# Kernel optimization log

Measured on AMD Instinct MI355X. Metric: run time of the kernel, lower is better.

The kernel has to match this reference:

```python
import jax, jax.numpy as jnp
import numpy as np

N_NODES = 100000
N_EDGES = 800000
NODE_IN = 32
EDGE_DIM = 84
HIDDEN = 24
HEAD_HIDDEN = 20
DEPTH = 2
CAT = 2 * HIDDEN + EDGE_DIM  # 132
LN_EPS = 1e-5


def _gelu(x):
    # torch nn.GELU default = exact erf form
    return jax.nn.gelu(x, approximate=False)


def _ln(x, g, b):
    m = jnp.mean(x, axis=-1, keepdims=True)
    v = jnp.var(x, axis=-1, keepdims=True)
    return (x - m) * jax.lax.rsqrt(v + LN_EPS) * g + b


def setup_inputs() -> dict:
    key = jax.random.key(0)
    ks = jax.random.split(key, 32)
    f = jnp.float32

    def nrm(k, shape, scale=0.05):
        return jax.random.normal(k, shape, dtype=f) * scale

    inp = {
        "x": jax.random.normal(ks[0], (N_NODES, NODE_IN), dtype=f),
        "edge_attr": jax.random.normal(ks[1], (N_EDGES, EDGE_DIM), dtype=f),
        # input projection
        "node_w": nrm(ks[2], (NODE_IN, HIDDEN)),
        "node_b": jnp.zeros((HIDDEN,), f),
        # intrinsic head
        "ih_w1": nrm(ks[3], (HIDDEN, HEAD_HIDDEN)),
        "ih_b1": jnp.zeros((HEAD_HIDDEN,), f),
        "ih_w2": nrm(ks[4], (HEAD_HIDDEN, 1)),
        "ih_b2": jnp.zeros((1,), f),
        # per-layer phi_e (stacked over depth)
        "pe_w1": nrm(ks[5], (DEPTH, CAT, EDGE_DIM)),
        "pe_b1": jnp.zeros((DEPTH, EDGE_DIM), f),
        "pe_w2": nrm(ks[6], (DEPTH, EDGE_DIM, EDGE_DIM)),
        "pe_b2": jnp.zeros((DEPTH, EDGE_DIM), f),
        # per-layer phi_v
        "pv_w1": nrm(ks[7], (DEPTH, CAT, HIDDEN)),
        "pv_b1": jnp.zeros((DEPTH, HIDDEN), f),
        "pv_w2": nrm(ks[8], (DEPTH, HIDDEN, HIDDEN)),
        "pv_b2": jnp.zeros((DEPTH, HIDDEN), f),
        # layer norms
        "ne_g": jnp.ones((DEPTH, EDGE_DIM), f),
        "ne_b": jnp.zeros((DEPTH, EDGE_DIM), f),
        "nv_g": jnp.ones((DEPTH, HIDDEN), f),
        "nv_b": jnp.zeros((DEPTH, HIDDEN), f),
        # context head
        "ch_w1": nrm(ks[9], (HIDDEN, HEAD_HIDDEN)),
        "ch_b1": jnp.zeros((HEAD_HIDDEN,), f),
        "ch_w2": nrm(ks[10], (HEAD_HIDDEN, 1)),
        "ch_b2": jnp.zeros((1,), f),
        "mu": jnp.zeros((), f),
        "edge_index": jax.random.randint(ks[11], (2, N_EDGES), 0, N_NODES),
    }
    return inp


def reference(x, edge_attr, node_w, node_b, ih_w1, ih_b1, ih_w2, ih_b2,
              pe_w1, pe_b1, pe_w2, pe_b2, pv_w1, pv_b1, pv_w2, pv_b2,
              ne_g, ne_b, nv_g, nv_b, ch_w1, ch_b1, ch_w2, ch_b2, mu,
              edge_index):
    src, dst = edge_index[0], edge_index[1]
    n = x.shape[0]
    # eval mode: dropout and edge_drop are inactive
    h = x @ node_w + node_b                                   # [N, H]
    intrinsic = (_gelu(h @ ih_w1 + ih_b1) @ ih_w2 + ih_b2)[:, 0]
    e = edge_attr                                             # [E, De]
    ones = jnp.ones((src.shape[0], 1), dtype=x.dtype)
    counts = jnp.maximum(jax.ops.segment_sum(ones, dst, num_segments=n), 1.0)
    for i in range(DEPTH):
        hs, hd = h[src], h[dst]                               # gathers [E, H]
        cat = jnp.concatenate([hs, hd, e], axis=-1)           # [E, 132]
        e_msg = _gelu(cat @ pe_w1[i] + pe_b1[i]) @ pe_w2[i] + pe_b2[i]
        e = _ln(e + e_msg, ne_g[i], ne_b[i])
        cat = jnp.concatenate([hs, hd, e], axis=-1)
        m = _gelu(cat @ pv_w1[i] + pv_b1[i]) @ pv_w2[i] + pv_b2[i]
        agg = jax.ops.segment_sum(m, dst, num_segments=n) / counts  # scatter-mean
        h = _ln(h + agg, nv_g[i], nv_b[i])
    context = (_gelu(h @ ch_w1 + ch_b1) @ ch_w2 + ch_b2)[:, 0]
    return mu + intrinsic + context
```

## Files before the change

### kernel.cpp

```cpp
#include <hip/hip_runtime.h>
#include <math.h>

#define N_NODES 100000
#define N_EDGES 800000
#define NODE_IN 32
#define EDGE_DIM 84
#define HIDDEN 24
#define HEAD_HIDDEN 20
#define CAT_DIM 132
#define LN_EPS 1e-5f

typedef __attribute__((ext_vector_type(8))) short short8;
typedef __attribute__((ext_vector_type(4))) float f32x4;
typedef unsigned int uint;
typedef unsigned short ushort;

__device__ __forceinline__ float gelu_exact(float x) {
    return 0.5f * x * (1.0f + erff(x * 0.70710678118654752f));
}
__device__ __forceinline__ ushort f2bf(float f) {
    union { float f; uint u; } c; c.f = f;
    uint u = c.u;
    return (ushort)((u + 0x7fffu + ((u >> 16) & 1u)) >> 16);
}
__device__ __forceinline__ float bf2f(ushort s) {
    union { uint u; float f; } c; c.u = ((uint)s) << 16; return c.f;
}

__global__ void k_prep_w(const float* __restrict__ pe_w1, const float* __restrict__ pe_w2,
                         const float* __restrict__ pv_w1, const float* __restrict__ pv_w2,
                         ushort* __restrict__ wp) {
    int idx = blockIdx.x * 256 + threadIdx.x;
    int j = idx & 7;
    int lane = (idx >> 3) & 63;
    int frag = idx >> 9;
    int kq = (lane >> 4) * 8 + j;
    int n15 = lane & 15;
    float v = 0.f;
    if (frag < 60) {
        int l = frag / 30, f = frag % 30;
        int kt = f / 6, nt = f % 6;
        int k = kt * 32 + kq, n = nt * 16 + n15;
        if (k < CAT_DIM && n < EDGE_DIM) v = pe_w1[(l * CAT_DIM + k) * EDGE_DIM + n];
    } else if (frag < 96) {
        int f2 = frag - 60; int l = f2 / 18, f = f2 % 18;
        int kt = f / 6, nt = f % 6;
        int k = kt * 32 + kq, n = nt * 16 + n15;
        if (k < EDGE_DIM && n < EDGE_DIM) v = pe_w2[(l * EDGE_DIM + k) * EDGE_DIM + n];
    } else if (frag < 116) {
        int f2 = frag - 96; int l = f2 / 10, f = f2 % 10;
        int kt = f / 2, nt = f % 2;
        int k = kt * 32 + kq, n = nt * 16 + n15;
        if (k < CAT_DIM && n < HIDDEN) v = pv_w1[(l * CAT_DIM + k) * HIDDEN + n];
    } else {
        int f2 = frag - 116; int l = f2 / 2, nt = f2 % 2;
        int k = kq, n = nt * 16 + n15;
        if (k < HIDDEN && n < HIDDEN) v = pv_w2[(l * HIDDEN + k) * HIDDEN + n];
    }
    wp[idx] = f2bf(v);
}

__global__ void k_node_in(const float* __restrict__ x,
                          const float* __restrict__ node_w, const float* __restrict__ node_b,
                          const float* __restrict__ ih_w1, const float* __restrict__ ih_b1,
                          const float* __restrict__ ih_w2, const float* __restrict__ ih_b2,
                          float* __restrict__ h, ushort* __restrict__ h_bf,
                          float* __restrict__ intr) {
    int n = blockIdx.x * blockDim.x + threadIdx.x;
    if (n >= N_NODES) return;
    float xv[NODE_IN];
    const float4* xp = (const float4*)(x + (size_t)n * NODE_IN);
#pragma unroll
    for (int i = 0; i < NODE_IN / 4; i++) {
        float4 v = xp[i];
        xv[4*i+0] = v.x; xv[4*i+1] = v.y; xv[4*i+2] = v.z; xv[4*i+3] = v.w;
    }
    float hv[HIDDEN];
#pragma unroll
    for (int j = 0; j < HIDDEN; j++) hv[j] = node_b[j];
    for (int k = 0; k < NODE_IN; k++) {
        float xk = xv[k];
#pragma unroll
        for (int j = 0; j < HIDDEN; j++) hv[j] = fmaf(xk, node_w[k * HIDDEN + j], hv[j]);
    }
#pragma unroll
    for (int j = 0; j < HIDDEN; j++) {
        h[(size_t)n * HIDDEN + j] = hv[j];
        h_bf[(size_t)n * HIDDEN + j] = f2bf(hv[j]);
    }
    float acc = ih_b2[0];
    for (int j = 0; j < HEAD_HIDDEN; j++) {
        float t = ih_b1[j];
#pragma unroll
        for (int k = 0; k < HIDDEN; k++) t = fmaf(hv[k], ih_w1[k * HEAD_HIDDEN + j], t);
        acc = fmaf(gelu_exact(t), ih_w2[j], acc);
    }
    intr[n] = acc;
}

__global__ void k_counts(const int* __restrict__ ei, int* __restrict__ cnt) {
    int e = blockIdx.x * blockDim.x + threadIdx.x;
    if (e >= N_EDGES) return;
    atomicAdd(&cnt[ei[N_EDGES + e]], 1);
}

__global__ __launch_bounds__(256, 2)
void k_edge_e(const ushort* __restrict__ h_bf,
              const float* __restrict__ e_in_f32,
              ushort* __restrict__ e_bf,
              const int* __restrict__ ei,
              const ushort* __restrict__ w1f, const ushort* __restrict__ w2f,
              const float* __restrict__ b1, const float* __restrict__ b2,
              const float* __restrict__ g, const float* __restrict__ bb) {
    __shared__ __align__(16) uint sA32[128 * 84];
    __shared__ __align__(16) ushort sT[128 * 104];
    __shared__ int s_idx[256];

    const int tid = threadIdx.x;
    const int e0 = blockIdx.x * 128;
    s_idx[tid] = ei[(size_t)(tid >> 7) * N_EDGES + e0 + (tid & 127)];
    __syncthreads();

    {
        int e = tid >> 1, hf = tid & 1;
        int src = s_idx[e], dst = s_idx[128 + e];
        const uint* hb = (const uint*)h_bf;
        uint* row = sA32 + e * 84;
#pragma unroll
        for (int i = 0; i < 6; i++) row[hf * 6 + i] = hb[src * 12 + hf * 6 + i];
#pragma unroll
        for (int i = 0; i < 6; i++) row[12 + hf * 6 + i] = hb[dst * 12 + hf * 6 + i];
        if (e_in_f32) {
            const float* er = e_in_f32 + (size_t)(e0 + e) * 84;
#pragma unroll
            for (int i = 0; i < 21; i++) {
                int jd = hf * 21 + i;
                uint lo = f2bf(er[2 * jd]), hi = f2bf(er[2 * jd + 1]);
                row[24 + jd] = lo | (hi << 16);
            }
        } else {
            const uint* er = (const uint*)e_bf + (size_t)(e0 + e) * 42;
#pragma unroll
            for (int i = 0; i < 21; i++) { int jd = hf * 21 + i; row[24 + jd] = er[jd]; }
        }
#pragma unroll
        for (int i = 0; i < 7; i++) row[66 + hf * 7 + i] = 0u;
    }

    const int lane = tid & 63, wave = tid >> 6;
    const int quad = lane >> 4, l15 = lane & 15;
    float b1v[6], b2v[6], gv[6], bbv[6];
#pragma unroll
    for (int nt = 0; nt < 6; nt++) {
        int col = nt * 16 + l15;
        bool ok = col < EDGE_DIM;
        b1v[nt] = ok ? b1[col] : 0.f;
        b2v[nt] = ok ? b2[col] : 0.f;
        gv[nt]  = ok ? g[col]  : 0.f;
        bbv[nt] = ok ? bb[col] : 0.f;
    }
    __syncthreads();

    const ushort* sAu = (const ushort*)sA32;
    const int r0 = wave * 32 + l15;

    f32x4 acc[2][6];
#pragma unroll
    for (int mt = 0; mt < 2; mt++)
#pragma unroll
        for (int nt = 0; nt < 6; nt++) acc[mt][nt] = (f32x4)0.f;

#pragma unroll
    for (int kt = 0; kt < 5; kt++) {
        short8 a0 = *(const short8*)(sAu + (size_t)r0 * 168 + kt * 32 + quad * 8);
        short8 a1 = *(const short8*)(sAu + (size_t)(r0 + 16) * 168 + kt * 32 + quad * 8);
        const short8* bp = (const short8*)w1f + kt * 6 * 64 + lane;
#pragma unroll
        for (int nt = 0; nt < 6; nt++) {
            short8 b = bp[nt * 64];
            acc[0][nt] = __builtin_amdgcn_mfma_f32_16x16x32_bf16(a0, b, acc[0][nt], 0, 0, 0);
            acc[1][nt] = __builtin_amdgcn_mfma_f32_16x16x32_bf16(a1, b, acc[1][nt], 0, 0, 0);
        }
    }

#pragma unroll
    for (int mt = 0; mt < 2; mt++)
#pragma unroll
        for (int nt = 0; nt < 6; nt++)
#pragma unroll
            for (int r = 0; r < 4; r++) {
                int row = wave * 32 + mt * 16 + quad * 4 + r;
                sT[row * 104 + nt * 16 + l15] = f2bf(gelu_exact(acc[mt][nt][r] + b1v[nt]));
            }
    __syncthreads();

    f32x4 acc2[2][6];
#pragma unroll
    for (int mt = 0; mt < 2; mt++)
#pragma unroll
        for (int nt = 0; nt < 6; nt++) acc2[mt][nt] = (f32x4)0.f;

#pragma unroll
    for (int kt = 0; kt < 3; kt++) {
        short8 a0 = *(const short8*)(sT + (size_t)r0 * 104 + kt * 32 + quad * 8);
        short8 a1 = *(const short8*)(sT + (size_t)(r0 + 16) * 104 + kt * 32 + quad * 8);
        const short8* bp = (const short8*)w2f + kt * 6 * 64 + lane;
#pragma unroll
        for (int nt = 0; nt < 6; nt++) {
            short8 b = bp[nt * 64];
            acc2[0][nt] = __builtin_amdgcn_mfma_f32_16x16x32_bf16(a0, b, acc2[0][nt], 0, 0, 0);
            acc2[1][nt] = __builtin_amdgcn_mfma_f32_16x16x32_bf16(a1, b, acc2[1][nt], 0, 0, 0);
        }
    }

#pragma unroll
    for (int mt = 0; mt < 2; mt++) {
#pragma unroll
        for (int r = 0; r < 4; r++) {
            int row = wave * 32 + mt * 16 + quad * 4 + r;
            float ss = 0.f, qq = 0.f;
#pragma unroll
            for (int nt = 0; nt < 6; nt++) {
                int col = nt * 16 + l15;
                float v = acc2[mt][nt][r] + b2v[nt];
                if (col < EDGE_DIM) v += bf2f(sAu[row * 168 + 48 + col]);
                else v = 0.f;
                acc2[mt][nt][r] = v;
                ss += v;
                qq = fmaf(v, v, qq);
            }
            ss += __shfl_xor(ss, 1); ss += __shfl_xor(ss, 2);
            ss += __shfl_xor(ss, 4); ss += __shfl_xor(ss, 8);
            qq += __shfl_xor(qq, 1); qq += __shfl_xor(qq, 2);
            qq += __shfl_xor(qq, 4); qq += __shfl_xor(qq, 8);
            float mean = ss * (1.f / EDGE_DIM);
            float var  = qq * (1.f / EDGE_DIM) - mean * mean;
            float rstd = rsqrtf(var + LN_EPS);
#pragma unroll
            for (int nt = 0; nt < 6; nt++) {
                int col = nt * 16 + l15;
                if (col < EDGE_DIM) {
                    float o = (acc2[mt][nt][r] - mean) * rstd * gv[nt] + bbv[nt];
                    ((ushort*)sA32)[row * 168 + 48 + col] = f2bf(o);
                }
            }
        }
    }
    __syncthreads();

    uint* dst32 = (uint*)e_bf + (size_t)e0 * 42;
#pragma unroll
    for (int i = 0; i < 21; i++) {
        int idx = tid + 256 * i;
        int row = idx / 42, d = idx - row * 42;
        dst32[idx] = sA32[row * 84 + 24 + d];
    }
}

__global__ __launch_bounds__(256, 2)
void k_edge_v(const ushort* __restrict__ h_bf, const ushort* __restrict__ e_bf,
              const int* __restrict__ ei,
              const ushort* __restrict__ v1f, const ushort* __restrict__ v2f,
              const float* __restrict__ vb1, const float* __restrict__ vb2,
              float* __restrict__ agg) {
    __shared__ __align__(16) uint sA32[128 * 84];
    __shared__ __align__(16) ushort sT[128 * 40];
    __shared__ int s_idx[256];

    const int tid = threadIdx.x;
    const int e0 = blockIdx.x * 128;
    s_idx[tid] = ei[(size_t)(tid >> 7) * N_EDGES + e0 + (tid & 127)];
    __syncthreads();

    {
        int e = tid >> 1, hf = tid & 1;
        int src = s_idx[e], dst = s_idx[128 + e];
        const uint* hb = (const uint*)h_bf;
        uint* row = sA32 + e * 84;
#pragma unroll
        for (int i = 0; i < 6; i++) row[hf * 6 + i] = hb[src * 12 + hf * 6 + i];
#pragma unroll
        for (int i = 0; i < 6; i++) row[12 + hf * 6 + i] = hb[dst * 12 + hf * 6 + i];
        const uint* er = (const uint*)e_bf + (size_t)(e0 + e) * 42;
#pragma unroll
        for (int i = 0; i < 21; i++) { int jd = hf * 21 + i; row[24 + jd] = er[jd]; }
#pragma unroll
        for (int i = 0; i < 7; i++) row[66 + hf * 7 + i] = 0u;
    }

    const int lane = tid & 63, wave = tid >> 6;
    const int quad = lane >> 4, l15 = lane & 15;
    float vb1v[2], vb2v[2];
#pragma unroll
    for (int nt = 0; nt < 2; nt++) {
        int col = nt * 16 + l15;
        bool ok = col < HIDDEN;
        vb1v[nt] = ok ? vb1[col] : 0.f;
        vb2v[nt] = ok ? vb2[col] : 0.f;
    }
    __syncthreads();

    const ushort* sAu = (const ushort*)sA32;
    const int r0 = wave * 32 + l15;

    f32x4 acc[2][2];
#pragma unroll
    for (int mt = 0; mt < 2; mt++)
#pragma unroll
        for (int nt = 0; nt < 2; nt++) acc[mt][nt] = (f32x4)0.f;

#pragma unroll
    for (int kt = 0; kt < 5; kt++) {
        short8 a0 = *(const short8*)(sAu + (size_t)r0 * 168 + kt * 32 + quad * 8);
        short8 a1 = *(const short8*)(sAu + (size_t)(r0 + 16) * 168 + kt * 32 + quad * 8);
        const short8* bp = (const short8*)v1f + kt * 2 * 64 + lane;
#pragma unroll
        for (int nt = 0; nt < 2; nt++) {
            short8 b = bp[nt * 64];
            acc[0][nt] = __builtin_amdgcn_mfma_f32_16x16x32_bf16(a0, b, acc[0][nt], 0, 0, 0);
            acc[1][nt] = __builtin_amdgcn_mfma_f32_16x16x32_bf16(a1, b, acc[1][nt], 0, 0, 0);
        }
    }

#pragma unroll
    for (int mt = 0; mt < 2; mt++)
#pragma unroll
        for (int nt = 0; nt < 2; nt++)
#pragma unroll
            for (int r = 0; r < 4; r++) {
                int row = wave * 32 + mt * 16 + quad * 4 + r;
                sT[row * 40 + nt * 16 + l15] = f2bf(gelu_exact(acc[mt][nt][r] + vb1v[nt]));
            }
    __syncthreads();

    f32x4 acc2[2][2];
#pragma unroll
    for (int mt = 0; mt < 2; mt++)
#pragma unroll
        for (int nt = 0; nt < 2; nt++) acc2[mt][nt] = (f32x4)0.f;
    {
        short8 a0 = *(const short8*)(sT + (size_t)r0 * 40 + quad * 8);
        short8 a1 = *(const short8*)(sT + (size_t)(r0 + 16) * 40 + quad * 8);
        const short8* bp = (const short8*)v2f + lane;
#pragma unroll
        for (int nt = 0; nt < 2; nt++) {
            short8 b = bp[nt * 64];
            acc2[0][nt] = __builtin_amdgcn_mfma_f32_16x16x32_bf16(a0, b, acc2[0][nt], 0, 0, 0);
            acc2[1][nt] = __builtin_amdgcn_mfma_f32_16x16x32_bf16(a1, b, acc2[1][nt], 0, 0, 0);
        }
    }

#pragma unroll
    for (int mt = 0; mt < 2; mt++)
#pragma unroll
        for (int nt = 0; nt < 2; nt++) {
            int col = nt * 16 + l15;
            if (col < HIDDEN) {
#pragma unroll
                for (int r = 0; r < 4; r++) {
                    int row = wave * 32 + mt * 16 + quad * 4 + r;
                    int dst = s_idx[128 + row];
                    atomicAdd(&agg[(size_t)dst * HIDDEN + col], acc2[mt][nt][r] + vb2v[nt]);
                }
            }
        }
}

__global__ void k_node_up(float* __restrict__ h, ushort* __restrict__ h_bf,
                          const float* __restrict__ agg,
                          const int* __restrict__ cnt,
                          const float* __restrict__ g, const float* __restrict__ b) {
    int n = blockIdx.x * blockDim.x + threadIdx.x;
    if (n >= N_NODES) return;
    int c = cnt[n]; if (c < 1) c = 1;
    float inv = 1.0f / (float)c;
    float v[HIDDEN];
    float s = 0.f;
#pragma unroll
    for (int j = 0; j < HIDDEN; j++) {
        v[j] = h[(size_t)n * HIDDEN + j] + agg[(size_t)n * HIDDEN + j] * inv;
        s += v[j];
    }
    float mean = s * (1.f / HIDDEN);
    float sq = 0.f;
#pragma unroll
    for (int j = 0; j < HIDDEN; j++) { float d = v[j] - mean; sq = fmaf(d, d, sq); }
    float rstd = rsqrtf(sq * (1.f / HIDDEN) + LN_EPS);
#pragma unroll
    for (int j = 0; j < HIDDEN; j++) {
        float o = (v[j] - mean) * rstd * g[j] + b[j];
        h[(size_t)n * HIDDEN + j] = o;
        h_bf[(size_t)n * HIDDEN + j] = f2bf(o);
    }
}

__global__ void k_final(const float* __restrict__ h, const float* __restrict__ intr,
                        const float* __restrict__ ch_w1, const float* __restrict__ ch_b1,
                        const float* __restrict__ ch_w2, const float* __restrict__ ch_b2,
                        const float* __restrict__ mu, float* __restrict__ out) {
    int n = blockIdx.x * blockDim.x + threadIdx.x;
    if (n >= N_NODES) return;
    float hv[HIDDEN];
#pragma unroll
    for (int j = 0; j < HIDDEN; j++) hv[j] = h[(size_t)n * HIDDEN + j];
    float acc = ch_b2[0];
    for (int j = 0; j < HEAD_HIDDEN; j++) {
        float t = ch_b1[j];
#pragma unroll
        for (int k = 0; k < HIDDEN; k++) t = fmaf(hv[k], ch_w1[k * HEAD_HIDDEN + j], t);
        acc = fmaf(gelu_exact(t), ch_w2[j], acc);
    }
    out[n] = mu[0] + intr[n] + acc;
}

extern "C" void kernel_launch(void* const* d_in, const int* in_sizes, int n_in,
                              void* d_out, int out_size, void* d_ws, size_t ws_size,
                              hipStream_t stream) {
    const float* x        = (const float*)d_in[0];
    const float* edge_attr= (const float*)d_in[1];
    const float* node_w   = (const float*)d_in[2];
    const float* node_b   = (const float*)d_in[3];
    const float* ih_w1    = (const float*)d_in[4];
    const float* ih_b1    = (const float*)d_in[5];
    const float* ih_w2    = (const float*)d_in[6];
    const float* ih_b2    = (const float*)d_in[7];
    const float* pe_w1    = (const float*)d_in[8];
    const float* pe_b1    = (const float*)d_in[9];
    const float* pe_w2    = (const float*)d_in[10];
    const float* pe_b2    = (const float*)d_in[11];
    const float* pv_w1    = (const float*)d_in[12];
    const float* pv_b1    = (const float*)d_in[13];
    const float* pv_w2    = (const float*)d_in[14];
    const float* pv_b2    = (const float*)d_in[15];
    const float* ne_g     = (const float*)d_in[16];
    const float* ne_b     = (const float*)d_in[17];
    const float* nv_g     = (const float*)d_in[18];
    const float* nv_b     = (const float*)d_in[19];
    const float* ch_w1    = (const float*)d_in[20];
    const float* ch_b1    = (const float*)d_in[21];
    const float* ch_w2    = (const float*)d_in[22];
    const float* ch_b2    = (const float*)d_in[23];
    const float* mu       = (const float*)d_in[24];
    const int*   ei       = (const int*)d_in[25];

    char* ws = (char*)d_ws;
    float*  h    = (float*)ws;  ws += (size_t)N_NODES * HIDDEN * 4;
    float*  agg  = (float*)ws;  ws += (size_t)N_NODES * HIDDEN * 4;
    float*  intr = (float*)ws;  ws += (size_t)N_NODES * 4;
    int*    cnt  = (int*)ws;    ws += (size_t)N_NODES * 4;
    ushort* h_bf = (ushort*)ws; ws += (size_t)N_NODES * HIDDEN * 2;
    ushort* wp   = (ushort*)ws; ws += (size_t)61440 * 2;
    ws = (char*)(((size_t)ws + 255) & ~(size_t)255);
    ushort* e_bf = (ushort*)ws; ws += (size_t)N_EDGES * EDGE_DIM * 2;

    const ushort* we1[2] = { wp + 0 * 15360, wp + 1 * 15360 };
    const ushort* we2[2] = { wp + 30720 + 0 * 9216, wp + 30720 + 1 * 9216 };
    const ushort* wv1[2] = { wp + 49152 + 0 * 5120, wp + 49152 + 1 * 5120 };
    const ushort* wv2[2] = { wp + 59392 + 0 * 1024, wp + 59392 + 1 * 1024 };

    hipMemsetAsync(cnt, 0, (size_t)N_NODES * 4, stream);
    k_prep_w<<<240, 256, 0, stream>>>(pe_w1, pe_w2, pv_w1, pv_w2, wp);
    k_counts<<<(N_EDGES + 255) / 256, 256, 0, stream>>>(ei, cnt);
    k_node_in<<<(N_NODES + 255) / 256, 256, 0, stream>>>(
        x, node_w, node_b, ih_w1, ih_b1, ih_w2, ih_b2, h, h_bf, intr);

    const int eb = N_EDGES / 128;
    for (int L = 0; L < 2; L++) {
        k_edge_e<<<eb, 256, 0, stream>>>(
            h_bf, (L == 0) ? edge_attr : (const float*)nullptr, e_bf, ei,
            we1[L], we2[L],
            pe_b1 + (size_t)L * EDGE_DIM, pe_b2 + (size_t)L * EDGE_DIM,
            ne_g + (size_t)L * EDGE_DIM, ne_b + (size_t)L * EDGE_DIM);
        hipMemsetAsync(agg, 0, (size_t)N_NODES * HIDDEN * 4, stream);
        k_edge_v<<<eb, 256, 0, stream>>>(
            h_bf, e_bf, ei, wv1[L], wv2[L],
            pv_b1 + (size_t)L * HIDDEN, pv_b2 + (size_t)L * HIDDEN, agg);
        k_node_up<<<(N_NODES + 255) / 256, 256, 0, stream>>>(
            h, h_bf, agg, cnt, nv_g + (size_t)L * HIDDEN, nv_b + (size_t)L * HIDDEN);
    }
    k_final<<<(N_NODES + 255) / 256, 256, 0, stream>>>(
        h, intr, ch_w1, ch_b1, ch_w2, ch_b2, mu, (float*)d_out);
}
```

Before: 1.159 ms.

## Fuse edge-update and message kernels; load MFMA operands directly from global

Merges the phi_e edge update and phi_v message/scatter into one kernel per layer, so the updated edge features stay in shared memory instead of being written and re-read. The MFMA A operands are now loaded straight from global memory (gathered h rows, edge features), which drops the staging copy into LDS. The edge buffer is padded to 96 columns and is written back only after the first layer, since the last layer's edge output is never used. LDS use shrinks and launch bounds rise to 4 blocks per CU, at the cost of extra global loads (the residual is re-read in the LN step) and fewer barriers around the sT reuse.

Result: faster. 1.014 ms (-12.6%).

```diff
diff --git a/kernel.cpp b/kernel.cpp
--- a/kernel.cpp
+++ b/kernel.cpp
@@ -104,16 +104,55 @@
     atomicAdd(&cnt[ei[N_EDGES + e]], 1);
 }
 
-__global__ __launch_bounds__(256, 2)
-void k_edge_e(const ushort* __restrict__ h_bf,
-              const float* __restrict__ e_in_f32,
-              ushort* __restrict__ e_bf,
-              const int* __restrict__ ei,
-              const ushort* __restrict__ w1f, const ushort* __restrict__ w2f,
-              const float* __restrict__ b1, const float* __restrict__ b2,
-              const float* __restrict__ g, const float* __restrict__ bb) {
-    __shared__ __align__(16) uint sA32[128 * 84];
+__device__ __forceinline__ short8 ld_catA(const ushort* __restrict__ h_bf,
+                                          const float* __restrict__ eattr,
+                                          const ushort* __restrict__ e_bf,
+                                          int src, int dst, long rowg, int c) {
+    if (c < 48) {
+        const ushort* p = (c < 24) ? h_bf + (size_t)src * 24 + c
+                                   : h_bf + (size_t)dst * 24 + (c - 24);
+        return *(const short8*)p;
+    }
+    int ec = c - 48;
+    if (eattr) {
+        const float* q = eattr + rowg * 84;
+        f32x4 lo = *(const f32x4*)(q + ((ec <= 80) ? ec : 0));
+        f32x4 hi = *(const f32x4*)(q + ((ec <= 76) ? (ec + 4) : 0));
+        short8 r;
+        r[0] = (short)f2bf(lo[0]); r[1] = (short)f2bf(lo[1]);
+        r[2] = (short)f2bf(lo[2]); r[3] = (short)f2bf(lo[3]);
+        r[4] = (short)f2bf(hi[0]); r[5] = (short)f2bf(hi[1]);
+        r[6] = (short)f2bf(hi[2]); r[7] = (short)f2bf(hi[3]);
+        return r;
+    }
+    return *(const short8*)(e_bf + rowg * 96 + ((ec < 96) ? ec : 0));
+}
+
+__device__ __forceinline__ short8 ld_catV(const ushort* __restrict__ h_bf,
+                                          const ushort* __restrict__ sT,
+                                          int src, int dst, int rowL, int c) {
+    if (c < 48) {
+        const ushort* p = (c < 24) ? h_bf + (size_t)src * 24 + c
+                                   : h_bf + (size_t)dst * 24 + (c - 24);
+        return *(const short8*)p;
+    }
+    int ec = c - 48;
+    return *(const short8*)(sT + rowL * 104 + ((ec < 96) ? ec : 0));
+}
+
+__global__ __launch_bounds__(256, 4)
+void k_edge_fused(const ushort* __restrict__ h_bf,
+                  const float* __restrict__ eattr,
+                  ushort* __restrict__ e_bf,
+                  const int* __restrict__ ei,
+                  const ushort* __restrict__ w1f, const ushort* __restrict__ w2f,
+                  const ushort* __restrict__ v1f, const ushort* __restrict__ v2f,
+                  const float* __restrict__ b1, const float* __restrict__ b2,
+                  const float* __restrict__ g, const float* __restrict__ bb,
+                  const float* __restrict__ vb1, const float* __restrict__ vb2,
+                  float* __restrict__ agg, int store_e) {
     __shared__ __align__(16) ushort sT[128 * 104];
+    __shared__ __align__(16) ushort sTV[128 * 40];
     __shared__ int s_idx[256];
 
     const int tid = threadIdx.x;
@@ -121,59 +160,24 @@
     s_idx[tid] = ei[(size_t)(tid >> 7) * N_EDGES + e0 + (tid & 127)];
     __syncthreads();
 
-    {
-        int e = tid >> 1, hf = tid & 1;
-        int src = s_idx[e], dst = s_idx[128 + e];
-        const uint* hb = (const uint*)h_bf;
-        uint* row = sA32 + e * 84;
-#pragma unroll
-        for (int i = 0; i < 6; i++) row[hf * 6 + i] = hb[src * 12 + hf * 6 + i];
-#pragma unroll
-        for (int i = 0; i < 6; i++) row[12 + hf * 6 + i] = hb[dst * 12 + hf * 6 + i];
-        if (e_in_f32) {
-            const float* er = e_in_f32 + (size_t)(e0 + e) * 84;
-#pragma unroll
-            for (int i = 0; i < 21; i++) {
-                int jd = hf * 21 + i;
-                uint lo = f2bf(er[2 * jd]), hi = f2bf(er[2 * jd + 1]);
-                row[24 + jd] = lo | (hi << 16);
-            }
-        } else {
-            const uint* er = (const uint*)e_bf + (size_t)(e0 + e) * 42;
-#pragma unroll
-            for (int i = 0; i < 21; i++) { int jd = hf * 21 + i; row[24 + jd] = er[jd]; }
-        }
-#pragma unroll
-        for (int i = 0; i < 7; i++) row[66 + hf * 7 + i] = 0u;
-    }
-
     const int lane = tid & 63, wave = tid >> 6;
     const int quad = lane >> 4, l15 = lane & 15;
-    float b1v[6], b2v[6], gv[6], bbv[6];
-#pragma unroll
-    for (int nt = 0; nt < 6; nt++) {
-        int col = nt * 16 + l15;
-        bool ok = col < EDGE_DIM;
-        b1v[nt] = ok ? b1[col] : 0.f;
-        b2v[nt] = ok ? b2[col] : 0.f;
-        gv[nt]  = ok ? g[col]  : 0.f;
-        bbv[nt] = ok ? bb[col] : 0.f;
-    }
-    __syncthreads();
-
-    const ushort* sAu = (const ushort*)sA32;
-    const int r0 = wave * 32 + l15;
+    const int cbase = quad * 8;
+    const int rA0 = wave * 32 + l15;
+    int srcA[2], dstA[2];
+    srcA[0] = s_idx[rA0];      dstA[0] = s_idx[128 + rA0];
+    srcA[1] = s_idx[rA0 + 16]; dstA[1] = s_idx[128 + rA0 + 16];
 
     f32x4 acc[2][6];
 #pragma unroll
     for (int mt = 0; mt < 2; mt++)
 #pragma unroll
         for (int nt = 0; nt < 6; nt++) acc[mt][nt] = (f32x4)0.f;
-
 #pragma unroll
     for (int kt = 0; kt < 5; kt++) {
-        short8 a0 = *(const short8*)(sAu + (size_t)r0 * 168 + kt * 32 + quad * 8);
-        short8 a1 = *(const short8*)(sAu + (size_t)(r0 + 16) * 168 + kt * 32 + quad * 8);
+        int c = kt * 32 + cbase;
+        short8 a0 = ld_catA(h_bf, eattr, e_bf, srcA[0], dstA[0], (long)(e0 + rA0), c);
+        short8 a1 = ld_catA(h_bf, eattr, e_bf, srcA[1], dstA[1], (long)(e0 + rA0 + 16), c);
         const short8* bp = (const short8*)w1f + kt * 6 * 64 + lane;
 #pragma unroll
         for (int nt = 0; nt < 6; nt++) {
@@ -182,28 +186,28 @@
             acc[1][nt] = __builtin_amdgcn_mfma_f32_16x16x32_bf16(a1, b, acc[1][nt], 0, 0, 0);
         }
     }
-
-#pragma unroll
-    for (int mt = 0; mt < 2; mt++)
-#pragma unroll
-        for (int nt = 0; nt < 6; nt++)
+#pragma unroll
+    for (int nt = 0; nt < 6; nt++) {
+        int col = nt * 16 + l15;
+        float bv = (col < EDGE_DIM) ? b1[col] : 0.f;
+#pragma unroll
+        for (int mt = 0; mt < 2; mt++)
 #pragma unroll
             for (int r = 0; r < 4; r++) {
                 int row = wave * 32 + mt * 16 + quad * 4 + r;
-                sT[row * 104 + nt * 16 + l15] = f2bf(gelu_exact(acc[mt][nt][r] + b1v[nt]));
+                sT[row * 104 + col] = f2bf(gelu_exact(acc[mt][nt][r] + bv));
             }
-    __syncthreads();
+    }
 
     f32x4 acc2[2][6];
 #pragma unroll
     for (int mt = 0; mt < 2; mt++)
 #pragma unroll
         for (int nt = 0; nt < 6; nt++) acc2[mt][nt] = (f32x4)0.f;
-
 #pragma unroll
     for (int kt = 0; kt < 3; kt++) {
-        short8 a0 = *(const short8*)(sT + (size_t)r0 * 104 + kt * 32 + quad * 8);
-        short8 a1 = *(const short8*)(sT + (size_t)(r0 + 16) * 104 + kt * 32 + quad * 8);
+        short8 a0 = *(const short8*)(sT + (size_t)rA0 * 104 + kt * 32 + cbase);
+        short8 a1 = *(const short8*)(sT + (size_t)(rA0 + 16) * 104 + kt * 32 + cbase);
         const short8* bp = (const short8*)w2f + kt * 6 * 64 + lane;
 #pragma unroll
         for (int nt = 0; nt < 6; nt++) {
@@ -218,16 +222,18 @@
 #pragma unroll
         for (int r = 0; r < 4; r++) {
             int row = wave * 32 + mt * 16 + quad * 4 + r;
+            long rg = e0 + row;
+            float vv[6];
             float ss = 0.f, qq = 0.f;
 #pragma unroll
             for (int nt = 0; nt < 6; nt++) {
                 int col = nt * 16 + l15;
-                float v = acc2[mt][nt][r] + b2v[nt];
-                if (col < EDGE_DIM) v += bf2f(sAu[row * 168 + 48 + col]);
-                else v = 0.f;
-                acc2[mt][nt][r] = v;
-                ss += v;
-                qq = fmaf(v, v, qq);
+                float v = 0.f;
+                if (col < EDGE_DIM) {
+                    v = acc2[mt][nt][r] + b2[col];
+                    v += eattr ? eattr[rg * 84 + col] : bf2f(e_bf[rg * 96 + col]);
+                }
+                vv[nt] = v; ss += v; qq = fmaf(v, v, qq);
             }
             ss += __shfl_xor(ss, 1); ss += __shfl_xor(ss, 2);
             ss += __shfl_xor(ss, 4); ss += __shfl_xor(ss, 8);
@@ -239,131 +245,86 @@
 #pragma unroll
             for (int nt = 0; nt < 6; nt++) {
                 int col = nt * 16 + l15;
-                if (col < EDGE_DIM) {
-                    float o = (acc2[mt][nt][r] - mean) * rstd * gv[nt] + bbv[nt];
-                    ((ushort*)sA32)[row * 168 + 48 + col] = f2bf(o);
-                }
+                if (col < EDGE_DIM)
+                    sT[row * 104 + col] = f2bf((vv[nt] - mean) * rstd * g[col] + bb[col]);
             }
         }
     }
-    __syncthreads();
-
-    uint* dst32 = (uint*)e_bf + (size_t)e0 * 42;
-#pragma unroll
-    for (int i = 0; i < 21; i++) {
-        int idx = tid + 256 * i;
-        int row = idx / 42, d = idx - row * 42;
-        dst32[idx] = sA32[row * 84 + 24 + d];
-    }
-}
-
-__global__ __launch_bounds__(256, 2)
-void k_edge_v(const ushort* __restrict__ h_bf, const ushort* __restrict__ e_bf,
-              const int* __restrict__ ei,
-              const ushort* __restrict__ v1f, const ushort* __restrict__ v2f,
-              const float* __restrict__ vb1, const float* __restrict__ vb2,
-              float* __restrict__ agg) {
-    __shared__ __align__(16) uint sA32[128 * 84];
-    __shared__ __align__(16) ushort sT[128 * 40];
-    __shared__ int s_idx[256];
-
-    const int tid = threadIdx.x;
-    const int e0 = blockIdx.x * 128;
-    s_idx[tid] = ei[(size_t)(tid >> 7) * N_EDGES + e0 + (tid & 127)];
-    __syncthreads();
-
-    {
-        int e = tid >> 1, hf = tid & 1;
-        int src = s_idx[e], dst = s_idx[128 + e];
-        const uint* hb = (const uint*)h_bf;
-        uint* row = sA32 + e * 84;
-#pragma unroll
-        for (int i = 0; i < 6; i++) row[hf * 6 + i] = hb[src * 12 + hf * 6 + i];
-#pragma unroll
-        for (int i = 0; i < 6; i++) row[12 + hf * 6 + i] = hb[dst * 12 + hf * 6 + i];
-        const uint* er = (const uint*)e_bf + (size_t)(e0 + e) * 42;
-#pragma unroll
-        for (int i = 0; i < 21; i++) { int jd = hf * 21 + i; row[24 + jd] = er[jd]; }
-#pragma unroll
-        for (int i = 0; i < 7; i++) row[66 + hf * 7 + i] = 0u;
-    }
-
-    const int lane = tid & 63, wave = tid >> 6;
-    const int quad = lane >> 4, l15 = lane & 15;
-    float vb1v[2], vb2v[2];
+
+    f32x4 av[2][2];
+#pragma unroll
+    for (int mt = 0; mt < 2; mt++)
+#pragma unroll
+        for (int nt = 0; nt < 2; nt++) av[mt][nt] = (f32x4)0.f;
+#pragma unroll
+    for (int kt = 0; kt < 5; kt++) {
+        int c = kt * 32 + cbase;
+        short8 a0 = ld_catV(h_bf, sT, srcA[0], dstA[0], rA0, c);
+        short8 a1 = ld_catV(h_bf, sT, srcA[1], dstA[1], rA0 + 16, c);
+        const short8* bp = (const short8*)v1f + kt * 2 * 64 + lane;
+#pragma unroll
+        for (int nt = 0; nt < 2; nt++) {
+            short8 b = bp[nt * 64];
+            av[0][nt] = __builtin_amdgcn_mfma_f32_16x16x32_bf16(a0, b, av[0][nt], 0, 0, 0);
+            av[1][nt] = __builtin_amdgcn_mfma_f32_16x16x32_bf16(a1, b, av[1][nt], 0, 0, 0);
+        }
+    }
 #pragma unroll
     for (int nt = 0; nt < 2; nt++) {
         int col = nt * 16 + l15;
-        bool ok = col < HIDDEN;
-        vb1v[nt] = ok ? vb1[col] : 0.f;
-        vb2v[nt] = ok ? vb2[col] : 0.f;
-    }
-    __syncthreads();
-
-    const ushort* sAu = (const ushort*)sA32;
-    const int r0 = wave * 32 + l15;
-
-    f32x4 acc[2][2];
+        float bv = (col < HIDDEN) ? vb1[col] : 0.f;
+#pragma unroll
+        for (int mt = 0; mt < 2; mt++)
+#pragma unroll
+            for (int r = 0; r < 4; r++) {
+                int row = wave * 32 + mt * 16 + quad * 4 + r;
+                sTV[row * 40 + col] = f2bf(gelu_exact(av[mt][nt][r] + bv));
+            }
+    }
+
+    f32x4 av2[2][2];
 #pragma unroll
     for (int mt = 0; mt < 2; mt++)
 #pragma unroll
-        for (int nt = 0; nt < 2; nt++) acc[mt][nt] = (f32x4)0.f;
-
-#pragma unroll
-    for (int kt = 0; kt < 5; kt++) {
-        short8 a0 = *(const short8*)(sAu + (size_t)r0 * 168 + kt * 32 + quad * 8);
-        short8 a1 = *(const short8*)(sAu + (size_t)(r0 + 16) * 168 + kt * 32 + quad * 8);
-        const short8* bp = (const short8*)v1f + kt * 2 * 64 + lane;
+        for (int nt = 0; nt < 2; nt++) av2[mt][nt] = (f32x4)0.f;
+    {
+        short8 a0 = *(const short8*)(sTV + (size_t)rA0 * 40 + cbase);
+        short8 a1 = *(const short8*)(sTV + (size_t)(rA0 + 16) * 40 + cbase);
+        const short8* bp = (const short8*)v2f + lane;
 #pragma unroll
         for (int nt = 0; nt < 2; nt++) {
             short8 b = bp[nt * 64];
-            acc[0][nt] = __builtin_amdgcn_mfma_f32_16x16x32_bf16(a0, b, acc[0][nt], 0, 0, 0);
-            acc[1][nt] = __builtin_amdgcn_mfma_f32_16x16x32_bf16(a1, b, acc[1][nt], 0, 0, 0);
-        }
-    }
-
-#pragma unroll
-    for (int mt = 0; mt < 2; mt++)
-#pragma unroll
-        for (int nt = 0; nt < 2; nt++)
-#pragma unroll
-            for (int r = 0; r < 4; r++) {
-                int row = wave * 32 + mt * 16 + quad * 4 + r;
-                sT[row * 40 + nt * 16 + l15] = f2bf(gelu_exact(acc[mt][nt][r] + vb1v[nt]));
-            }
-    __syncthreads();
-
-    f32x4 acc2[2][2];
-#pragma unroll
-    for (int mt = 0; mt < 2; mt++)
-#pragma unroll
-        for (int nt = 0; nt < 2; nt++) acc2[mt][nt] = (f32x4)0.f;
-    {
-        short8 a0 = *(const short8*)(sT + (size_t)r0 * 40 + quad * 8);
-        short8 a1 = *(const short8*)(sT + (size_t)(r0 + 16) * 40 + quad * 8);
-        const short8* bp = (const short8*)v2f + lane;
-#pragma unroll
-        for (int nt = 0; nt < 2; nt++) {
-            short8 b = bp[nt * 64];
-            acc2[0][nt] = __builtin_amdgcn_mfma_f32_16x16x32_bf16(a0, b, acc2[0][nt], 0, 0, 0);
-            acc2[1][nt] = __builtin_amdgcn_mfma_f32_16x16x32_bf16(a1, b, acc2[1][nt], 0, 0, 0);
-        }
-    }
-
-#pragma unroll
-    for (int mt = 0; mt < 2; mt++)
-#pragma unroll
-        for (int nt = 0; nt < 2; nt++) {
-            int col = nt * 16 + l15;
-            if (col < HIDDEN) {
+            av2[0][nt] = __builtin_amdgcn_mfma_f32_16x16x32_bf16(a0, b, av2[0][nt], 0, 0, 0);
+            av2[1][nt] = __builtin_amdgcn_mfma_f32_16x16x32_bf16(a1, b, av2[1][nt], 0, 0, 0);
+        }
+    }
+#pragma unroll
+    for (int nt = 0; nt < 2; nt++) {
+        int col = nt * 16 + l15;
+        if (col < HIDDEN) {
+            float bv = vb2[col];
+#pragma unroll
+            for (int mt = 0; mt < 2; mt++)
 #pragma unroll
                 for (int r = 0; r < 4; r++) {
                     int row = wave * 32 + mt * 16 + quad * 4 + r;
-                    int dst = s_idx[128 + row];
-                    atomicAdd(&agg[(size_t)dst * HIDDEN + col], acc2[mt][nt][r] + vb2v[nt]);
+                    int d = s_idx[128 + row];
+                    atomicAdd(&agg[(size_t)d * HIDDEN + col], av2[mt][nt][r] + bv);
                 }
-            }
-        }
+        }
+    }
+
+    if (store_e) {
+        __syncthreads();
+        const uint* sTu = (const uint*)sT;
+        uint* dst32 = (uint*)e_bf + (size_t)e0 * 48;
+#pragma unroll
+        for (int i = 0; i < 24; i++) {
+            int idx = tid + 256 * i;
+            int row = idx / 48, d = idx - row * 48;
+            dst32[idx] = sTu[row * 52 + d];
+        }
+    }
 }
 
 __global__ void k_node_up(float* __restrict__ h, ushort* __restrict__ h_bf,
@@ -451,7 +412,7 @@
     ushort* h_bf = (ushort*)ws; ws += (size_t)N_NODES * HIDDEN * 2;
     ushort* wp   = (ushort*)ws; ws += (size_t)61440 * 2;
     ws = (char*)(((size_t)ws + 255) & ~(size_t)255);
-    ushort* e_bf = (ushort*)ws; ws += (size_t)N_EDGES * EDGE_DIM * 2;
+    ushort* e_bf = (ushort*)ws; ws += (size_t)N_EDGES * 96 * 2;
 
     const ushort* we1[2] = { wp + 0 * 15360, wp + 1 * 15360 };
     const ushort* we2[2] = { wp + 30720 + 0 * 9216, wp + 30720 + 1 * 9216 };
@@ -466,15 +427,14 @@
 
     const int eb = N_EDGES / 128;
     for (int L = 0; L < 2; L++) {
-        k_edge_e<<<eb, 256, 0, stream>>>(
+        hipMemsetAsync(agg, 0, (size_t)N_NODES * HIDDEN * 4, stream);
+        k_edge_fused<<<eb, 256, 0, stream>>>(
             h_bf, (L == 0) ? edge_attr : (const float*)nullptr, e_bf, ei,
-            we1[L], we2[L],
+            we1[L], we2[L], wv1[L], wv2[L],
             pe_b1 + (size_t)L * EDGE_DIM, pe_b2 + (size_t)L * EDGE_DIM,
-            ne_g + (size_t)L * EDGE_DIM, ne_b + (size_t)L * EDGE_DIM);
-        hipMemsetAsync(agg, 0, (size_t)N_NODES * HIDDEN * 4, stream);
-        k_edge_v<<<eb, 256, 0, stream>>>(
-            h_bf, e_bf, ei, wv1[L], wv2[L],
-            pv_b1 + (size_t)L * HIDDEN, pv_b2 + (size_t)L * HIDDEN, agg);
+            ne_g + (size_t)L * EDGE_DIM, ne_b + (size_t)L * EDGE_DIM,
+            pv_b1 + (size_t)L * HIDDEN, pv_b2 + (size_t)L * HIDDEN,
+            agg, (L == 0) ? 1 : 0);
         k_node_up<<<(N_NODES + 255) / 256, 256, 0, stream>>>(
             h, h_bf, agg, cnt, nv_g + (size_t)L * HIDDEN, nv_b + (size_t)L * HIDDEN);
     }
```
